# Performance work log

Hardware: AMD Instinct MI355X
Metric: run time of the kernel (lower is better)

The kernel has to match this reference:

```python
import jax, jax.numpy as jnp
import numpy as np

R, S, D_IN, WIDTH, K = 8192, 128, 16, 64, 8  # rays, samples/ray, feat dim, net_width, net_kernels


def setup_inputs() -> dict:
    key = jax.random.key(0)
    ks = jax.random.split(key, 8)
    he = jax.nn.initializers.he_uniform()
    idxs = jax.random.randint(ks[0], (R, S), 0, K, dtype=jnp.int32)
    xs = jax.random.normal(ks[1], (R, S, D_IN), dtype=jnp.float32)
    # MultiMLP params: net_depth=2 hidden MultiDense layers + 1 output layer, each with K kernels
    W0 = he(ks[2], (K, D_IN, WIDTH), jnp.float32)
    b0 = jnp.zeros((K, WIDTH), jnp.float32)
    W1 = he(ks[3], (K, WIDTH, WIDTH), jnp.float32)
    b1 = jnp.zeros((K, WIDTH), jnp.float32)
    W2 = he(ks[4], (K, WIDTH, 1), jnp.float32)
    b2 = jnp.zeros((K, 1), jnp.float32)
    return {"idxs": idxs, "xs": xs, "W0": W0, "b0": b0, "W1": W1, "b1": b1, "W2": W2, "b2": b2}


def _multi_dense(idx, x, W, b):
    """Per-sample kernel select: out[n] = x[n] @ W[idx[n]] + b[idx[n]].

    x: [N, d], W: [K, d, f], b: [K, f], idx: [N] int. Loop is over the small
    fixed kernel count K (not a data dim); avoids materializing an [N, d, f]
    gathered-weight tensor.
    """
    out = jnp.zeros((x.shape[0], W.shape[-1]), x.dtype)
    zero = jnp.zeros((), x.dtype)
    for k in range(W.shape[0]):
        sel = (idx == k)[:, None]
        out = out + jnp.where(sel, x @ W[k] + b[k], zero)
    return out


def reference(idxs, xs, W0, b0, W1, b1, W2, b2):
    batch_shape = idxs.shape  # (R, S)
    idx = idxs.reshape(-1)
    h = xs.reshape(-1, xs.shape[-1])
    h = jax.nn.relu(_multi_dense(idx, h, W0, b0))
    h = jax.nn.relu(_multi_dense(idx, h, W1, b1))
    out = _multi_dense(idx, h, W2, b2)  # [N, 1] density
    return out.reshape(*batch_shape, 1)
```

## Files before the change

### kernel.cpp

```cpp
#include <hip/hip_runtime.h>
#include <hip/hip_bf16.h>


typedef __attribute__((ext_vector_type(8))) short bfrag;
typedef __attribute__((ext_vector_type(4))) float ffrag;

#define SPAN        512
#define NSPANS      2048
#define IMG_STRIDE  13312
#define WS_NEED     ((size_t)(8 * IMG_STRIDE))

__device__ __forceinline__ unsigned short bf16r(float f) {
    unsigned int u = __float_as_uint(f);
    u += 0x7fffu + ((u >> 16) & 1u);
    return (unsigned short)(u >> 16);
}
__device__ __forceinline__ unsigned int pack_trunc(float hiF, float loF) {
    return __builtin_amdgcn_perm(__float_as_uint(hiF), __float_as_uint(loF), 0x07060302u);
}
__device__ __forceinline__ unsigned int pack_cvt(float loF, float hiF) {
    union { __hip_bfloat162 h2; unsigned int u; } c;
    c.h2 = __float22bfloat162_rn(make_float2(loF, hiF));
    return c.u;
}

__global__ void k_build_images(const float* __restrict__ W0, const float* __restrict__ b0,
                               const float* __restrict__ W1, const float* __restrict__ b1,
                               const float* __restrict__ W2, const float* __restrict__ b2,
                               unsigned char* __restrict__ wsB) {
    const int k = blockIdx.x, t = threadIdx.x;
    unsigned char* img = wsB + k * IMG_STRIDE;
    unsigned short* w0b = (unsigned short*)img;
    unsigned short* w1b = (unsigned short*)(img + 4096);
    float* bias = (float*)(img + 12288);
    for (int e = t; e < 2048; e += 256) {
        int j = e & 7, lane = (e >> 3) & 63, nt = e >> 9, q = lane >> 4;
        int kk = q * 8 + j, n = nt * 16 + (lane & 15);
        unsigned short v = 0;
        if (kk < 16) v = bf16r(W0[k * 1024 + kk * 64 + n]);
        else if (kk == 16) v = bf16r(b0[k * 64 + n]);
        w0b[e] = v;
    }
    for (int e = t; e < 4096; e += 256) {
        int j = e & 7, lane = (e >> 3) & 63, s = (e >> 9) & 1, nt = e >> 10, q = lane >> 4;
        int h = (j & 3) * 16 + s * 8 + q * 2 + (j >> 2);
        w1b[e] = bf16r(W1[k * 4096 + h * 64 + nt * 16 + (lane & 15)]);
    }
    if (t < 64) bias[t] = b1[k * 64 + t];
    else if (t < 128) bias[t] = W2[k * 64 + (t - 64)];
    else if (t == 128) bias[128] = b2[k];
}

__global__ __launch_bounds__(256, 4) void k_fused(const int* __restrict__ idxs,
                                                  const float* __restrict__ xs,
                                                  const unsigned char* __restrict__ wsB,
                                                  float* __restrict__ out) {
    __shared__ int wcnt[2][4][8];
    __shared__ int bsbase[2][4][8];
    __shared__ int cntS[8], startS[8];
    __shared__ unsigned short sId[SPAN];
    __shared__ __align__(16) unsigned short Xg[SPAN * 16];
    __shared__ __align__(16) unsigned short H3[4][16 * 72];
    __shared__ float outBuf[SPAN];

    const int tid = threadIdx.x, lane = tid & 63, w = tid >> 6;
    const int q = lane >> 4, l15 = lane & 15;
    const int base = blockIdx.x * SPAN;

    const float4* xp0 = (const float4*)(xs + (size_t)(base + tid) * 16);
    const float4* xp1 = (const float4*)(xs + (size_t)(base + 256 + tid) * 16);
    float4 g0 = xp0[0], g1 = xp0[1], g2 = xp0[2], g3 = xp0[3];
    float4 g4 = xp1[0], g5 = xp1[1], g6 = xp1[2], g7 = xp1[3];

    int kreg[2], lrank[2];
    #pragma unroll
    for (int it = 0; it < 2; ++it) {
        int k = idxs[base + it * 256 + tid];
        kreg[it] = k;
        unsigned long long mymask = 0;
        #pragma unroll
        for (int kk = 0; kk < 8; ++kk) {
            unsigned long long m = __ballot(k == kk);
            if (k == kk) mymask = m;
            if (lane == 0) wcnt[it][w][kk] = (int)__popcll(m);
        }
        lrank[it] = (int)__popcll(mymask & ((1ull << lane) - 1ull));
    }
    __syncthreads();
    if (tid < 8) {
        int c = 0;
        for (int it = 0; it < 2; ++it)
            for (int w2 = 0; w2 < 4; ++w2) c += wcnt[it][w2][tid];
        cntS[tid] = c;
    }
    __syncthreads();
    if (tid == 0) {
        int s = 0;
        for (int k = 0; k < 8; ++k) { startS[k] = s; s += cntS[k]; }
    }
    __syncthreads();
    if (tid < 64) {
        int it = tid >> 5, w2 = (tid >> 3) & 3, kk = tid & 7;
        int b = startS[kk];
        for (int it2 = 0; it2 < it; ++it2)
            for (int w3 = 0; w3 < 4; ++w3) b += wcnt[it2][w3][kk];
        for (int w3 = 0; w3 < w2; ++w3) b += wcnt[it][w3][kk];
        bsbase[it][w2][kk] = b;
    }
    __syncthreads();
    #pragma unroll
    for (int it = 0; it < 2; ++it)
        sId[bsbase[it][w][kreg[it]] + lrank[it]] = (unsigned short)(it * 256 + tid);

    {
        uint4 lo, hi;
        lo.x = pack_trunc(g0.y, g0.x); lo.y = pack_trunc(g0.w, g0.z);
        lo.z = pack_trunc(g1.y, g1.x); lo.w = pack_trunc(g1.w, g1.z);
        hi.x = pack_trunc(g2.y, g2.x); hi.y = pack_trunc(g2.w, g2.z);
        hi.z = pack_trunc(g3.y, g3.x); hi.w = pack_trunc(g3.w, g3.z);
        *(uint4*)(Xg + tid * 16) = lo;
        *(uint4*)(Xg + tid * 16 + 8) = hi;
        lo.x = pack_trunc(g4.y, g4.x); lo.y = pack_trunc(g4.w, g4.z);
        lo.z = pack_trunc(g5.y, g5.x); lo.w = pack_trunc(g5.w, g5.z);
        hi.x = pack_trunc(g6.y, g6.x); hi.y = pack_trunc(g6.w, g6.z);
        hi.z = pack_trunc(g7.y, g7.x); hi.w = pack_trunc(g7.w, g7.z);
        *(uint4*)(Xg + (256 + tid) * 16) = lo;
        *(uint4*)(Xg + (256 + tid) * 16 + 8) = hi;
    }
    __syncthreads();

    unsigned short* H = H3[w];
    #pragma unroll
    for (int kk2 = 0; kk2 < 2; ++kk2) {
        const int k = w + kk2 * 4;
        const int cnt = cntS[k];
        if (cnt == 0) continue;
        const int start = startS[k];
        const unsigned char* img = wsB + k * IMG_STRIDE;

        bfrag w0f[4], w1f[4][2];
        #pragma unroll
        for (int nt = 0; nt < 4; ++nt)
            w0f[nt] = *(const bfrag*)(img + nt * 1024 + lane * 16);
        #pragma unroll
        for (int nt = 0; nt < 4; ++nt)
            #pragma unroll
            for (int s = 0; s < 2; ++s)
                w1f[nt][s] = *(const bfrag*)(img + 4096 + ((nt * 2 + s) * 64 + lane) * 16);
        const float* bias = (const float*)(img + 12288);
        float b1v[4], w2v[4];
        #pragma unroll
        for (int nt = 0; nt < 4; ++nt) {
            b1v[nt] = bias[nt * 16 + l15];
            w2v[nt] = bias[64 + nt * 16 + l15];
        }
        const float b2v = bias[128];

        const int nst = (cnt + 15) >> 4;

        auto loadA = [&](int st, bfrag* a, int* rowid) {
            int R = start + st * 16 + l15;
            int Rm = start + cnt - 1;
            R = R < Rm ? R : Rm;
            int row = (int)sId[R];
            *rowid = row;
            bfrag av = {0, 0, 0, 0, 0, 0, 0, 0};
            if (q < 2)
                av = *(const bfrag*)(Xg + row * 16 + q * 8);
            else if (q == 2)
                av[0] = (short)0x3F80;
            *a = av;
        };

        bfrag aCur;
        int rowCur;
        loadA(0, &aCur, &rowCur);

        for (int st = 0; st < nst; ++st) {
            ffrag acc0[4];
            #pragma unroll
            for (int nt = 0; nt < 4; ++nt) {
                ffrag z = {0.f, 0.f, 0.f, 0.f};
                acc0[nt] = __builtin_amdgcn_mfma_f32_16x16x32_bf16(aCur, w0f[nt], z, 0, 0, 0);
            }
            bfrag aNxt = {0, 0, 0, 0, 0, 0, 0, 0};
            int rowNxt = 0;
            if (st + 1 < nst) loadA(st + 1, &aNxt, &rowNxt);

            #pragma unroll
            for (int r = 0; r < 4; ++r) {
                float v0 = acc0[0][r]; v0 = v0 > 0.f ? v0 : 0.f;
                float v1 = acc0[1][r]; v1 = v1 > 0.f ? v1 : 0.f;
                float v2 = acc0[2][r]; v2 = v2 > 0.f ? v2 : 0.f;
                float v3 = acc0[3][r]; v3 = v3 > 0.f ? v3 : 0.f;
                uint2 u;
                u.x = pack_cvt(v0, v1);
                u.y = pack_cvt(v2, v3);
                *(uint2*)((unsigned char*)H + (q * 4 + r) * 144 + l15 * 8) = u;
            }

            bfrag a10 = *(const bfrag*)((unsigned char*)H + l15 * 144 + q * 16);
            bfrag a11 = *(const bfrag*)((unsigned char*)H + l15 * 144 + 64 + q * 16);
            ffrag acc1[4];
            #pragma unroll
            for (int nt = 0; nt < 4; ++nt) {
                ffrag z = {0.f, 0.f, 0.f, 0.f};
                acc1[nt] = __builtin_amdgcn_mfma_f32_16x16x32_bf16(a10, w1f[nt][0], z, 0, 0, 0);
                acc1[nt] = __builtin_amdgcn_mfma_f32_16x16x32_bf16(a11, w1f[nt][1], acc1[nt], 0, 0, 0);
            }

            #pragma unroll
            for (int r = 0; r < 4; ++r) {
                float p = 0.f;
                #pragma unroll
                for (int nt = 0; nt < 4; ++nt) {
                    float h = acc1[nt][r] + b1v[nt];
                    h = h > 0.f ? h : 0.f;
                    p = fmaf(h, w2v[nt], p);
                }
                p += __shfl_xor(p, 1);
                p += __shfl_xor(p, 2);
                p += __shfl_xor(p, 4);
                p += __shfl_xor(p, 8);
                if (l15 == q * 4 + r && st * 16 + l15 < cnt)
                    outBuf[rowCur] = p + b2v;
            }

            aCur = aNxt;
            rowCur = rowNxt;
        }
    }
    __syncthreads();

    ((float2*)(out + base))[tid] = ((const float2*)outBuf)[tid];
}

__global__ void k_fallback(const int* __restrict__ idxs, const float* __restrict__ xs,
                           const float* __restrict__ W0, const float* __restrict__ b0,
                           const float* __restrict__ W1, const float* __restrict__ b1,
                           const float* __restrict__ W2, const float* __restrict__ b2,
                           float* __restrict__ out, int N) {
    int n = blockIdx.x * blockDim.x + threadIdx.x;
    if (n >= N) return;
    int k = idxs[n];
    float h0[64];
    #pragma unroll
    for (int j = 0; j < 64; ++j) h0[j] = b0[k * 64 + j];
    for (int i = 0; i < 16; ++i) {
        float xi = xs[(size_t)n * 16 + i];
        #pragma unroll
        for (int j = 0; j < 64; ++j) h0[j] = fmaf(xi, W0[k * 1024 + i * 64 + j], h0[j]);
    }
    #pragma unroll
    for (int j = 0; j < 64; ++j) h0[j] = fmaxf(h0[j], 0.f);
    float acc = b2[k];
    for (int jc = 0; jc < 4; ++jc) {
        float h1[16];
        #pragma unroll
        for (int j = 0; j < 16; ++j) h1[j] = b1[k * 64 + jc * 16 + j];
        for (int i = 0; i < 64; ++i) {
            float hv = h0[i];
            #pragma unroll
            for (int j = 0; j < 16; ++j)
                h1[j] = fmaf(hv, W1[k * 4096 + i * 64 + jc * 16 + j], h1[j]);
        }
        #pragma unroll
        for (int j = 0; j < 16; ++j) acc = fmaf(fmaxf(h1[j], 0.f), W2[k * 64 + jc * 16 + j], acc);
    }
    out[n] = acc;
}

extern "C" void kernel_launch(void* const* d_in, const int* in_sizes, int n_in,
                              void* d_out, int out_size, void* d_ws, size_t ws_size,
                              hipStream_t stream) {
    const int*   idxs = (const int*)d_in[0];
    const float* xs   = (const float*)d_in[1];
    const float* W0   = (const float*)d_in[2];
    const float* b0   = (const float*)d_in[3];
    const float* W1   = (const float*)d_in[4];
    const float* b1   = (const float*)d_in[5];
    const float* W2   = (const float*)d_in[6];
    const float* b2   = (const float*)d_in[7];
    float* out = (float*)d_out;
    const int N = in_sizes[0];

    if (N != SPAN * NSPANS || ws_size < WS_NEED) {
        k_fallback<<<(N + 255) / 256, 256, 0, stream>>>(idxs, xs, W0, b0, W1, b1, W2, b2, out, N);
        return;
    }

    unsigned char* wsB = (unsigned char*)d_ws;
    k_build_images<<<8, 256, 0, stream>>>(W0, b0, W1, b1, W2, b2, wsB);
    k_fused<<<NSPANS, 256, 0, stream>>>(idxs, xs, wsB, out);
}
```

Before: 143.7 us.

## Scatter inputs into kernel-sorted LDS layout and compute output layer with MFMA

The converted bf16 inputs are now written directly into kernel-sorted, fragment-friendly tile order in LDS, so the MLP loop reads contiguous rows instead of gathering through an index. The final 64->1 layer becomes a pair of MFMAs with a zero-padded W2 image, replacing the per-row shuffle reduction, and b1 is folded into the MFMA accumulator init. Shared memory is packed into one aliased buffer, the output staging buffer and final barrier are dropped in favour of direct scattered global stores, and launch bounds rise to 6 blocks per CU. The costs are an extra LDS round trip for the second hidden layer, scattered 4-byte global writes, and the removal of the software prefetch of the next A tile.

Result: slower. 218.0 us (+51.7%).

```diff
diff --git a/kernel.cpp b/kernel.cpp
--- a/kernel.cpp
+++ b/kernel.cpp
@@ -7,8 +7,14 @@
 
 #define SPAN        512
 #define NSPANS      2048
-#define IMG_STRIDE  13312
+#define IMG_STRIDE  15360
 #define WS_NEED     ((size_t)(8 * IMG_STRIDE))
+
+#define XG_B    0
+#define H3_B    16384
+#define SID_B   25088
+#define CNT_B   26112
+#define SMEM_SZ 26176
 
 __device__ __forceinline__ unsigned short bf16r(float f) {
     unsigned int u = __float_as_uint(f);
@@ -32,7 +38,8 @@
     unsigned char* img = wsB + k * IMG_STRIDE;
     unsigned short* w0b = (unsigned short*)img;
     unsigned short* w1b = (unsigned short*)(img + 4096);
-    float* bias = (float*)(img + 12288);
+    unsigned short* w2b = (unsigned short*)(img + 12288);
+    float* bias = (float*)(img + 14336);
     for (int e = t; e < 2048; e += 256) {
         int j = e & 7, lane = (e >> 3) & 63, nt = e >> 9, q = lane >> 4;
         int kk = q * 8 + j, n = nt * 16 + (lane & 15);
@@ -46,22 +53,26 @@
         int h = (j & 3) * 16 + s * 8 + q * 2 + (j >> 2);
         w1b[e] = bf16r(W1[k * 4096 + h * 64 + nt * 16 + (lane & 15)]);
     }
+    for (int e = t; e < 1024; e += 256) {
+        int j = e & 7, lane = (e >> 3) & 63, s = e >> 9, q = lane >> 4, l15 = lane & 15;
+        int h = (j & 3) * 16 + s * 8 + q * 2 + (j >> 2);
+        w2b[e] = (l15 == 0) ? bf16r(W2[k * 64 + h]) : (unsigned short)0;
+    }
     if (t < 64) bias[t] = b1[k * 64 + t];
-    else if (t < 128) bias[t] = W2[k * 64 + (t - 64)];
-    else if (t == 128) bias[128] = b2[k];
-}
-
-__global__ __launch_bounds__(256, 4) void k_fused(const int* __restrict__ idxs,
+    else if (t == 64) bias[64] = b2[k];
+}
+
+__global__ __launch_bounds__(256, 6) void k_fused(const int* __restrict__ idxs,
                                                   const float* __restrict__ xs,
                                                   const unsigned char* __restrict__ wsB,
                                                   float* __restrict__ out) {
-    __shared__ int wcnt[2][4][8];
-    __shared__ int bsbase[2][4][8];
-    __shared__ int cntS[8], startS[8];
-    __shared__ unsigned short sId[SPAN];
-    __shared__ __align__(16) unsigned short Xg[SPAN * 16];
-    __shared__ __align__(16) unsigned short H3[4][16 * 72];
-    __shared__ float outBuf[SPAN];
+    __shared__ __align__(16) unsigned char smem[SMEM_SZ];
+    unsigned short* Xg = (unsigned short*)(smem + XG_B);
+    unsigned short* sId = (unsigned short*)(smem + SID_B);
+    int* cntS = (int*)(smem + CNT_B);
+    int* startS = cntS + 8;
+    int* wcnt = (int*)(smem + H3_B);
+    int* bsbase = wcnt + 64;
 
     const int tid = threadIdx.x, lane = tid & 63, w = tid >> 6;
     const int q = lane >> 4, l15 = lane & 15;
@@ -82,15 +93,14 @@
         for (int kk = 0; kk < 8; ++kk) {
             unsigned long long m = __ballot(k == kk);
             if (k == kk) mymask = m;
-            if (lane == 0) wcnt[it][w][kk] = (int)__popcll(m);
+            if (lane == 0) wcnt[(it * 4 + w) * 8 + kk] = (int)__popcll(m);
         }
         lrank[it] = (int)__popcll(mymask & ((1ull << lane) - 1ull));
     }
     __syncthreads();
     if (tid < 8) {
         int c = 0;
-        for (int it = 0; it < 2; ++it)
-            for (int w2 = 0; w2 < 4; ++w2) c += wcnt[it][w2][tid];
+        for (int e = 0; e < 8; ++e) c += wcnt[e * 8 + tid];
         cntS[tid] = c;
     }
     __syncthreads();
@@ -102,15 +112,15 @@
     if (tid < 64) {
         int it = tid >> 5, w2 = (tid >> 3) & 3, kk = tid & 7;
         int b = startS[kk];
-        for (int it2 = 0; it2 < it; ++it2)
-            for (int w3 = 0; w3 < 4; ++w3) b += wcnt[it2][w3][kk];
-        for (int w3 = 0; w3 < w2; ++w3) b += wcnt[it][w3][kk];
-        bsbase[it][w2][kk] = b;
-    }
-    __syncthreads();
-    #pragma unroll
-    for (int it = 0; it < 2; ++it)
-        sId[bsbase[it][w][kreg[it]] + lrank[it]] = (unsigned short)(it * 256 + tid);
+        for (int e = 0; e < it * 4 + w2; ++e) b += wcnt[e * 8 + kk];
+        bsbase[(it * 4 + w2) * 8 + kk] = b;
+    }
+    __syncthreads();
+
+    int dest0 = bsbase[w * 8 + kreg[0]] + lrank[0];
+    int dest1 = bsbase[(4 + w) * 8 + kreg[1]] + lrank[1];
+    sId[dest0] = (unsigned short)tid;
+    sId[dest1] = (unsigned short)(256 + tid);
 
     {
         uint4 lo, hi;
@@ -118,18 +128,21 @@
         lo.z = pack_trunc(g1.y, g1.x); lo.w = pack_trunc(g1.w, g1.z);
         hi.x = pack_trunc(g2.y, g2.x); hi.y = pack_trunc(g2.w, g2.z);
         hi.z = pack_trunc(g3.y, g3.x); hi.w = pack_trunc(g3.w, g3.z);
-        *(uint4*)(Xg + tid * 16) = lo;
-        *(uint4*)(Xg + tid * 16 + 8) = hi;
+        int g = dest0 >> 4, m = dest0 & 15;
+        *(uint4*)(Xg + g * 256 + m * 8)       = lo;
+        *(uint4*)(Xg + g * 256 + 128 + m * 8) = hi;
         lo.x = pack_trunc(g4.y, g4.x); lo.y = pack_trunc(g4.w, g4.z);
         lo.z = pack_trunc(g5.y, g5.x); lo.w = pack_trunc(g5.w, g5.z);
         hi.x = pack_trunc(g6.y, g6.x); hi.y = pack_trunc(g6.w, g6.z);
         hi.z = pack_trunc(g7.y, g7.x); hi.w = pack_trunc(g7.w, g7.z);
-        *(uint4*)(Xg + (256 + tid) * 16) = lo;
-        *(uint4*)(Xg + (256 + tid) * 16 + 8) = hi;
-    }
-    __syncthreads();
-
-    unsigned short* H = H3[w];
+        g = dest1 >> 4; m = dest1 & 15;
+        *(uint4*)(Xg + g * 256 + m * 8)       = lo;
+        *(uint4*)(Xg + g * 256 + 128 + m * 8) = hi;
+    }
+    __syncthreads();
+
+    unsigned char* H = smem + H3_B + w * 2176;
+    const ffrag z = {0.f, 0.f, 0.f, 0.f};
     #pragma unroll
     for (int kk2 = 0; kk2 < 2; ++kk2) {
         const int k = w + kk2 * 4;
@@ -138,7 +151,7 @@
         const int start = startS[k];
         const unsigned char* img = wsB + k * IMG_STRIDE;
 
-        bfrag w0f[4], w1f[4][2];
+        bfrag w0f[4], w1f[4][2], w2f[2];
         #pragma unroll
         for (int nt = 0; nt < 4; ++nt)
             w0f[nt] = *(const bfrag*)(img + nt * 1024 + lane * 16);
@@ -147,45 +160,30 @@
             #pragma unroll
             for (int s = 0; s < 2; ++s)
                 w1f[nt][s] = *(const bfrag*)(img + 4096 + ((nt * 2 + s) * 64 + lane) * 16);
-        const float* bias = (const float*)(img + 12288);
-        float b1v[4], w2v[4];
-        #pragma unroll
-        for (int nt = 0; nt < 4; ++nt) {
-            b1v[nt] = bias[nt * 16 + l15];
-            w2v[nt] = bias[64 + nt * 16 + l15];
-        }
-        const float b2v = bias[128];
+        #pragma unroll
+        for (int s = 0; s < 2; ++s)
+            w2f[s] = *(const bfrag*)(img + 12288 + (s * 64 + lane) * 16);
+        const float* bias = (const float*)(img + 14336);
+        float b1v[4];
+        #pragma unroll
+        for (int nt = 0; nt < 4; ++nt) b1v[nt] = bias[nt * 16 + l15];
+        const float b2v = bias[64];
 
         const int nst = (cnt + 15) >> 4;
-
-        auto loadA = [&](int st, bfrag* a, int* rowid) {
+        for (int st = 0; st < nst; ++st) {
             int R = start + st * 16 + l15;
             int Rm = start + cnt - 1;
             R = R < Rm ? R : Rm;
-            int row = (int)sId[R];
-            *rowid = row;
-            bfrag av = {0, 0, 0, 0, 0, 0, 0, 0};
+            bfrag a = {0, 0, 0, 0, 0, 0, 0, 0};
             if (q < 2)
-                av = *(const bfrag*)(Xg + row * 16 + q * 8);
+                a = *(const bfrag*)(Xg + (R >> 4) * 256 + q * 128 + (R & 15) * 8);
             else if (q == 2)
-                av[0] = (short)0x3F80;
-            *a = av;
-        };
-
-        bfrag aCur;
-        int rowCur;
-        loadA(0, &aCur, &rowCur);
-
-        for (int st = 0; st < nst; ++st) {
+                a[0] = (short)0x3F80;
+
             ffrag acc0[4];
             #pragma unroll
-            for (int nt = 0; nt < 4; ++nt) {
-                ffrag z = {0.f, 0.f, 0.f, 0.f};
-                acc0[nt] = __builtin_amdgcn_mfma_f32_16x16x32_bf16(aCur, w0f[nt], z, 0, 0, 0);
-            }
-            bfrag aNxt = {0, 0, 0, 0, 0, 0, 0, 0};
-            int rowNxt = 0;
-            if (st + 1 < nst) loadA(st + 1, &aNxt, &rowNxt);
+            for (int nt = 0; nt < 4; ++nt)
+                acc0[nt] = __builtin_amdgcn_mfma_f32_16x16x32_bf16(a, w0f[nt], z, 0, 0, 0);
 
             #pragma unroll
             for (int r = 0; r < 4; ++r) {
@@ -196,43 +194,48 @@
                 uint2 u;
                 u.x = pack_cvt(v0, v1);
                 u.y = pack_cvt(v2, v3);
-                *(uint2*)((unsigned char*)H + (q * 4 + r) * 144 + l15 * 8) = u;
-            }
-
-            bfrag a10 = *(const bfrag*)((unsigned char*)H + l15 * 144 + q * 16);
-            bfrag a11 = *(const bfrag*)((unsigned char*)H + l15 * 144 + 64 + q * 16);
+                *(uint2*)(H + (q * 4 + r) * 136 + l15 * 8) = u;
+            }
+
+            bfrag a10 = *(const bfrag*)(H + l15 * 136 + q * 16);
+            bfrag a11 = *(const bfrag*)(H + l15 * 136 + 64 + q * 16);
             ffrag acc1[4];
             #pragma unroll
             for (int nt = 0; nt < 4; ++nt) {
-                ffrag z = {0.f, 0.f, 0.f, 0.f};
-                acc1[nt] = __builtin_amdgcn_mfma_f32_16x16x32_bf16(a10, w1f[nt][0], z, 0, 0, 0);
+                ffrag c1 = {b1v[nt], b1v[nt], b1v[nt], b1v[nt]};
+                acc1[nt] = __builtin_amdgcn_mfma_f32_16x16x32_bf16(a10, w1f[nt][0], c1, 0, 0, 0);
                 acc1[nt] = __builtin_amdgcn_mfma_f32_16x16x32_bf16(a11, w1f[nt][1], acc1[nt], 0, 0, 0);
             }
 
             #pragma unroll
             for (int r = 0; r < 4; ++r) {
-                float p = 0.f;
+                float v0 = acc1[0][r]; v0 = v0 > 0.f ? v0 : 0.f;
+                float v1 = acc1[1][r]; v1 = v1 > 0.f ? v1 : 0.f;
+                float v2 = acc1[2][r]; v2 = v2 > 0.f ? v2 : 0.f;
+                float v3 = acc1[3][r]; v3 = v3 > 0.f ? v3 : 0.f;
+                uint2 u;
+                u.x = pack_cvt(v0, v1);
+                u.y = pack_cvt(v2, v3);
+                *(uint2*)(H + (q * 4 + r) * 136 + l15 * 8) = u;
+            }
+
+            bfrag a20 = *(const bfrag*)(H + l15 * 136 + q * 16);
+            bfrag a21 = *(const bfrag*)(H + l15 * 136 + 64 + q * 16);
+            ffrag d = __builtin_amdgcn_mfma_f32_16x16x32_bf16(a20, w2f[0], z, 0, 0, 0);
+            d = __builtin_amdgcn_mfma_f32_16x16x32_bf16(a21, w2f[1], d, 0, 0, 0);
+
+            if (l15 == 0) {
                 #pragma unroll
-                for (int nt = 0; nt < 4; ++nt) {
-                    float h = acc1[nt][r] + b1v[nt];
-                    h = h > 0.f ? h : 0.f;
-                    p = fmaf(h, w2v[nt], p);
+                for (int r = 0; r < 4; ++r) {
+                    int row = st * 16 + q * 4 + r;
+                    if (row < cnt) {
+                        int oid = (int)sId[start + row];
+                        out[base + oid] = d[r] + b2v;
+                    }
                 }
-                p += __shfl_xor(p, 1);
-                p += __shfl_xor(p, 2);
-                p += __shfl_xor(p, 4);
-                p += __shfl_xor(p, 8);
-                if (l15 == q * 4 + r && st * 16 + l15 < cnt)
-                    outBuf[rowCur] = p + b2v;
-            }
-
-            aCur = aNxt;
-            rowCur = rowNxt;
+            }
         }
     }
-    __syncthreads();
-
-    ((float2*)(out + base))[tid] = ((const float2*)outBuf)[tid];
 }
 
 __global__ void k_fallback(const int* __restrict__ idxs, const float* __restrict__ xs,
```
